# Optimization experiments

Hardware: AMD Instinct MI355X
Metric: run time of the kernel (lower is better)

The kernel has to match this reference:

```python
import jax, jax.numpy as jnp
import numpy as np

H = 1024  # hidden_size == input_size


def setup_inputs() -> dict:
    key = jax.random.key(0)
    ks = jax.random.split(key, 12)
    B, T, S, I = 64, 128, 256, 1024
    sc_in = 1.0 / np.sqrt(I)
    sc_h = 1.0 / np.sqrt(H)
    return {
        "trg_emb": jax.random.normal(ks[0], (B, T, I), jnp.float32),
        "h0": jax.random.normal(ks[1], (B, H), jnp.float32),
        "c0": jax.random.normal(ks[2], (B, H), jnp.float32),
        "ctx": jax.random.normal(ks[3], (B, S, H), jnp.float32),
        "src_len": jax.random.randint(ks[4], (B,), 1, S + 1, jnp.int32),
        # nn.LSTM params (gate order i, f, g, o)
        "W_ih": jax.random.uniform(ks[5], (4 * H, I), jnp.float32, -sc_h, sc_h),
        "W_hh": jax.random.uniform(ks[6], (4 * H, H), jnp.float32, -sc_h, sc_h),
        "b_ih": jax.random.uniform(ks[7], (4 * H,), jnp.float32, -sc_h, sc_h),
        "b_hh": jax.random.uniform(ks[8], (4 * H,), jnp.float32, -sc_h, sc_h),
        # GlobalAttention (Luong general): linear_in (H->H), linear_out (2H->H), no bias
        "W_in": jax.random.uniform(ks[9], (H, H), jnp.float32, -sc_h, sc_h),
        "W_out": jax.random.uniform(ks[10], (H, 2 * H), jnp.float32, -sc_h, sc_h),
    }


def _lstm_scan(trg_emb, h0, c0, W_ih, W_hh, b_ih, b_hh):
    # Precompute input contributions for all steps: [B,T,4H] -> scan over T
    x_gates = jnp.einsum('bti,gi->btg', trg_emb, W_ih) + b_ih + b_hh

    def step(carry, xg):
        h, c = carry
        gates = xg + h @ W_hh.T  # [B,4H]
        i, f, g, o = jnp.split(gates, 4, axis=-1)
        c = jax.nn.sigmoid(f) * c + jax.nn.sigmoid(i) * jnp.tanh(g)
        h = jax.nn.sigmoid(o) * jnp.tanh(c)
        return (h, c), h

    (hT, cT), hs = jax.lax.scan(step, (h0, c0), jnp.swapaxes(x_gates, 0, 1))
    return jnp.swapaxes(hs, 0, 1), hT, cT  # [B,T,H], [B,H], [B,H]


def reference(trg_emb, h0, c0, ctx, src_len, W_ih, W_hh, b_ih, b_hh, W_in, W_out):
    # input_feed=False: LSTM recurrence is independent of attention -> run once,
    # then batch the global attention over all T timesteps (same math as the loop).
    lstm_out, hT, cT = _lstm_scan(trg_emb, h0, c0, W_ih, W_hh, b_ih, b_hh)

    q = jnp.einsum('bth,gh->btg', lstm_out, W_in)          # linear_in
    scores = jnp.einsum('bth,bsh->bts', q, ctx)            # [B,T,S]
    mask = jnp.arange(ctx.shape[1])[None, None, :] < src_len[:, None, None]
    scores = jnp.where(mask, scores, -jnp.inf)
    attn = jax.nn.softmax(scores, axis=-1)                 # att_dropout=0
    context = jnp.einsum('bts,bsh->bth', attn, ctx)        # [B,T,H]
    h_tilde = jnp.tanh(
        jnp.einsum('btc,hc->bth', jnp.concatenate([context, lstm_out], axis=-1), W_out)
    )  # [B,T,H]
    return h_tilde, (hT[None], cT[None])
```

## Files before the change

### kernel.cpp

```cpp
#include <hip/hip_runtime.h>
#include <math.h>

#define BB 64
#define TT 128
#define SS 256
#define HHH 1024

typedef unsigned short u16;
typedef unsigned int u32;
typedef unsigned long long u64t;
typedef __bf16 bf16x8 __attribute__((ext_vector_type(8)));
typedef float f32x4 __attribute__((ext_vector_type(4)));
typedef u16 u16x8 __attribute__((ext_vector_type(8)));

__device__ __forceinline__ float sigmoidf_(float x) { return 1.0f / (1.0f + expf(-x)); }
__device__ __forceinline__ u16 f2bf(float f) {
    __bf16 h = (__bf16)f;
    return __builtin_bit_cast(u16, h);
}
__device__ __forceinline__ float b2f(u16 u) {
    return __builtin_bit_cast(float, (u32)u << 16);
}
template <typename OT>
__device__ __forceinline__ void stout(OT* p, float v) {
    if constexpr (sizeof(OT) == 2) *p = f2bf(v); else *p = v;
}
__device__ __forceinline__ void astore(u64t* p, u64t v) {
    __hip_atomic_store(p, v, __ATOMIC_RELAXED, __HIP_MEMORY_SCOPE_AGENT);
}
__device__ __forceinline__ int afetchadd(int* p) {
    return __hip_atomic_fetch_add(p, 1, __ATOMIC_RELAXED, __HIP_MEMORY_SCOPE_AGENT);
}
__device__ __forceinline__ int aload32(const int* p) {
    return __hip_atomic_load(p, __ATOMIC_RELAXED, __HIP_MEMORY_SCOPE_AGENT);
}
__device__ __forceinline__ void astore32(int* p, int v) {
    __hip_atomic_store(p, v, __ATOMIC_RELAXED, __HIP_MEMORY_SCOPE_AGENT);
}
#define GLOAD16(gsrc, ldst)                                                      \
    __builtin_amdgcn_global_load_lds(                                            \
        (const __attribute__((address_space(1))) unsigned int*)(const void*)(gsrc), \
        (__attribute__((address_space(3))) unsigned int*)(void*)(ldst), 16, 0, 0)

__global__ __launch_bounds__(256) void convert_all(
    const float* __restrict__ trg, const float* __restrict__ wih,
    const float* __restrict__ win, const float* __restrict__ wout,
    u16* __restrict__ trg16, u16* __restrict__ wih16,
    u16* __restrict__ win16, u16* __restrict__ wout16)
{
    int b = blockIdx.x;
    const float* in;
    u16* out;
    long base;
    if (b < 4096)      { in = trg;  out = trg16;  base = (long)b * 2048; }
    else if (b < 6144) { in = wih;  out = wih16;  base = (long)(b - 4096) * 2048; }
    else if (b < 6656) { in = win;  out = win16;  base = (long)(b - 6144) * 2048; }
    else               { in = wout; out = wout16; base = (long)(b - 6656) * 2048; }
    long i = base + (long)threadIdx.x * 8;
    float4 a = *(const float4*)(in + i);
    float4 c = *(const float4*)(in + i + 4);
    u16x8 o;
    o[0] = f2bf(a.x); o[1] = f2bf(a.y); o[2] = f2bf(a.z); o[3] = f2bf(a.w);
    o[4] = f2bf(c.x); o[5] = f2bf(c.y); o[6] = f2bf(c.z); o[7] = f2bf(c.w);
    *(u16x8*)(out + i) = o;
}

__global__ __launch_bounds__(128) void wfrag_build(const float* __restrict__ W,
                                                   u16* __restrict__ WF) {
    const int w = blockIdx.x, kq = blockIdx.y, bid = blockIdx.z;
    const int t = threadIdx.x;
    const int rh = t >> 6, lane = t & 63;
    const int rowp = bid * 32 + rh * 16 + (lane & 15);
    const int g = rowp & 3, jrow = rowp >> 2;
    const int k = kq * 256 + w * 32 + (lane >> 4) * 8;
    const float* src = W + ((size_t)(g * 1024 + jrow) << 10) + k;
    float4 v0 = *(const float4*)src;
    float4 v1 = *(const float4*)(src + 4);
    float vv[8] = {v0.x, v0.y, v0.z, v0.w, v1.x, v1.y, v1.z, v1.w};
    u16x8 hi, lo;
#pragma unroll
    for (int i = 0; i < 8; ++i) {
        u16 h = f2bf(vv[i]);
        hi[i] = h;
        lo[i] = f2bf(vv[i] - b2f(h));
    }
    size_t fr = ((((size_t)bid * 4 + kq) * 8 + w) * 2 + rh) * 2;
    *(u16x8*)(WF + fr * 512 + (size_t)lane * 8) = hi;
    *(u16x8*)(WF + (fr + 1) * 512 + (size_t)lane * 8) = lo;
}

__global__ __launch_bounds__(256) void h0frag(const float* __restrict__ h0,
                                              u16* __restrict__ slot) {
    int i = blockIdx.x * 256 + threadIdx.x;
    int b = i >> 7, jg = i & 127;
    int j = jg << 3;
    const float* src = h0 + ((size_t)b << 10) + j;
    float4 v0 = *(const float4*)src;
    float4 v1 = *(const float4*)(src + 4);
    float vv[8] = {v0.x, v0.y, v0.z, v0.w, v1.x, v1.y, v1.z, v1.w};
    u16x8 hi, lo;
#pragma unroll
    for (int e = 0; e < 8; ++e) {
        u16 h = f2bf(vv[e]);
        hi[e] = h;
        lo[e] = f2bf(vv[e] - b2f(h));
    }
    int g = b >> 4, bl = b & 15;
    int kq = j >> 8, w = (j >> 5) & 7, tr = (j >> 3) & 3;
    int lane = tr * 16 + bl;
    size_t base = (size_t)g * 32768 + (size_t)((kq * 8 + w) * 2) * 512 + (size_t)lane * 8;
    *(u16x8*)(slot + base) = hi;
    *(u16x8*)(slot + base + 512) = lo;
}

template <bool TANH, bool XGT, typename OT>
__global__ __launch_bounds__(256) void gemm_mfma_bt(
    const u16* __restrict__ A0, const u16* __restrict__ A1,
    const u16* __restrict__ B, OT* __restrict__ C,
    int M, int N, int K, int KA0,
    const float* __restrict__ bias0, const float* __restrict__ bias1)
{
    __shared__ uint4 As4[512];
    __shared__ uint4 Bs4[512];
    u16* As = (u16*)As4;
    u16* Bs = (u16*)Bs4;
    const int tid = threadIdx.x;
    const int l = tid & 63;
    const int w = tid >> 6;
    const int wm = w >> 1, wn = w & 1;
    const int tc = l & 15, tr8 = (l >> 4) << 3;
    const int m0 = blockIdx.y << 7, n0 = blockIdx.x << 7;
    f32x4 acc[4][4] = {};

    for (int k0 = 0; k0 < K; k0 += 32) {
        const u16* Ap = (k0 < KA0) ? A0 : A1;
        const int koff = (k0 < KA0) ? k0 : k0 - KA0;
#pragma unroll
        for (int r = 0; r < 2; ++r) {
            int u = tid + (r << 8);
            int row = u >> 2, q = u & 3;
            size_t arow;
            if (XGT) {
                int rr = m0 + row;
                arow = (size_t)((rr & 63) * 128 + (rr >> 6));
            } else {
                arow = (size_t)(m0 + row);
            }
            GLOAD16(Ap + arow * KA0 + koff + (q << 3), &As4[u]);
            GLOAD16(B + (size_t)(n0 + row) * K + k0 + (q << 3), &Bs4[u]);
        }
        __syncthreads();
        bf16x8 bfr[4];
#pragma unroll
        for (int j = 0; j < 4; ++j)
            bfr[j] = *(const bf16x8*)(Bs + ((wn << 6) + (j << 4) + tc) * 32 + tr8);
#pragma unroll
        for (int i = 0; i < 4; ++i) {
            bf16x8 af = *(const bf16x8*)(As + ((wm << 6) + (i << 4) + tc) * 32 + tr8);
#pragma unroll
            for (int j = 0; j < 4; ++j)
                acc[i][j] = __builtin_amdgcn_mfma_f32_16x16x32_bf16(af, bfr[j], acc[i][j], 0, 0, 0);
        }
        __syncthreads();
    }
#pragma unroll
    for (int j = 0; j < 4; ++j) {
        const int col = n0 + (wn << 6) + (j << 4) + tc;
        const float bias = XGT ? (bias0[col] + bias1[col]) : 0.0f;
#pragma unroll
        for (int i = 0; i < 4; ++i) {
#pragma unroll
            for (int v = 0; v < 4; ++v) {
                int r = m0 + (wm << 6) + (i << 4) + ((l >> 4) << 2) + v;
                float val = acc[i][j][v];
                if (XGT) {
                    int newr = ((col & 1023) << 2) | (col >> 10);
                    ((float*)C)[(size_t)(r >> 6) * 262144 + (size_t)newr * 64 + (r & 63)] = val + bias;
                } else {
                    if (TANH) val = tanhf(val);
                    stout(&C[(size_t)r * N + col], val);
                }
            }
        }
    }
}

__global__ __launch_bounds__(512) void lstm_scan10(
    const float* __restrict__ xgt, const u16* __restrict__ WF,
    const float* __restrict__ c0,
    const u16* __restrict__ h0s, u16* __restrict__ ring,
    float* __restrict__ hT, float* __restrict__ cT,
    u16* __restrict__ lstm16, int* __restrict__ bar)
{
    __shared__ float red[4][64][17];
    __shared__ __align__(8) u16 tileh[16][16];
    __shared__ __align__(8) u16 tilel[16][16];
    const int tid = threadIdx.x;
    const int bid = blockIdx.x;
    const int g = bid >> 6;
    const int ib = bid & 63;
    const int kg = tid >> 6, l = tid & 63;
    const int kq = kg & 3, rh = kg >> 2;
    const int j0 = ib << 4;
    const int ebl = tid & 15;
    const int ejl = (tid >> 4) & 15;

    bf16x8 wfh[2][8], wfl[2][8];
#pragma unroll
    for (int rt = 0; rt < 2; ++rt) {
        const int R16 = ib * 4 + rh * 2 + rt;
        const int bw = R16 >> 1, rhw = R16 & 1;
#pragma unroll
        for (int w = 0; w < 8; ++w) {
            size_t fr = ((((size_t)bw * 4 + kq) * 8 + w) * 2 + rhw) * 2;
            wfh[rt][w] = *(const bf16x8*)(WF + fr * 512 + (size_t)l * 8);
            wfl[rt][w] = *(const bf16x8*)(WF + (fr + 1) * 512 + (size_t)l * 8);
        }
    }
    float cv = 0.0f;
    if (tid < 256) cv = c0[(size_t)(g * 16 + ebl) * 1024 + j0 + ejl];

    float xgvA[4] = {}, xgvB[4] = {};
    if (tid < 256) {
#pragma unroll
        for (int g2 = 0; g2 < 4; ++g2)
            xgvA[g2] = xgt[(size_t)(((j0 + ejl) << 2) + g2) * 64 + g * 16 + ebl];
    }

    const int kqs = ib >> 4, ws = (ib >> 1) & 7;
    int* const gbar = bar + (g << 9);

    for (int t = 0; t < 128; ++t) {
        const u16* hin = ((t == 0) ? h0s : (ring + (size_t)(t - 1) * 131072)) + (size_t)g * 32768;
        u16* hout = ring + (size_t)t * 131072 + (size_t)g * 32768;

        if (t < 127 && tid < 256) {
#pragma unroll
            for (int g2 = 0; g2 < 4; ++g2)
                xgvB[g2] = xgt[(size_t)(t + 1) * 262144 +
                               (size_t)(((j0 + ejl) << 2) + g2) * 64 + g * 16 + ebl];
        }

        f32x4 acc[2] = {};
        bf16x8 hbA[2], hbB[2];
#define LDW(HB, W)                                                                  \
        {                                                                           \
            size_t fb = (size_t)((kq * 8 + (W)) * 2) * 512 + (size_t)l * 8;         \
            HB[0] = *(const bf16x8*)(hin + fb);                                     \
            HB[1] = *(const bf16x8*)(hin + fb + 512);                               \
        }
        LDW(hbA, 0)
#pragma unroll
        for (int w = 0; w < 8; w += 2) {
            LDW(hbB, w + 1)
#pragma unroll
            for (int rt = 0; rt < 2; ++rt) {
                acc[rt] = __builtin_amdgcn_mfma_f32_16x16x32_bf16(wfh[rt][w], hbA[0], acc[rt], 0, 0, 0);
                acc[rt] = __builtin_amdgcn_mfma_f32_16x16x32_bf16(wfh[rt][w], hbA[1], acc[rt], 0, 0, 0);
                acc[rt] = __builtin_amdgcn_mfma_f32_16x16x32_bf16(wfl[rt][w], hbA[0], acc[rt], 0, 0, 0);
            }
            if (w + 2 < 8) LDW(hbA, w + 2)
#pragma unroll
            for (int rt = 0; rt < 2; ++rt) {
                acc[rt] = __builtin_amdgcn_mfma_f32_16x16x32_bf16(wfh[rt][w + 1], hbB[0], acc[rt], 0, 0, 0);
                acc[rt] = __builtin_amdgcn_mfma_f32_16x16x32_bf16(wfh[rt][w + 1], hbB[1], acc[rt], 0, 0, 0);
                acc[rt] = __builtin_amdgcn_mfma_f32_16x16x32_bf16(wfl[rt][w + 1], hbB[0], acc[rt], 0, 0, 0);
            }
        }
#undef LDW

#pragma unroll
        for (int rt = 0; rt < 2; ++rt)
#pragma unroll
            for (int v = 0; v < 4; ++v)
                red[kq][(rh << 5) + (rt << 4) + ((l >> 4) << 2) + v][l & 15] = acc[rt][v];
        __syncthreads();

        if (tid < 256) {
            float gate[4];
#pragma unroll
            for (int g2 = 0; g2 < 4; ++g2) {
                int rr = (ejl << 2) + g2;
                gate[g2] = red[0][rr][ebl] + red[1][rr][ebl] +
                           red[2][rr][ebl] + red[3][rr][ebl] + xgvA[g2];
            }
            float ii = sigmoidf_(gate[0]);
            float ff = sigmoidf_(gate[1]);
            float gg = tanhf(gate[2]);
            float oo = sigmoidf_(gate[3]);
            float cn = ff * cv + ii * gg;
            float hn = oo * tanhf(cn);
            cv = cn;
            u16 hh = f2bf(hn);
            tileh[ebl][ejl] = hh;
            tilel[ebl][ejl] = f2bf(hn - b2f(hh));
            if (t == 127) {
                hT[(size_t)(g * 16 + ebl) * 1024 + j0 + ejl] = hn;
                cT[(size_t)(g * 16 + ebl) * 1024 + j0 + ejl] = cn;
            }
        }
        __syncthreads();

        if (tid < 128) {
            const int plane = tid >> 6, rem = tid & 63;
            const int b2 = rem >> 2, half = (rem >> 1) & 1, qq = rem & 1;
            const int lane = ((ib & 1) * 2 + half) * 16 + b2;
            const u16* tp = plane ? &tilel[b2][half * 8 + qq * 4] : &tileh[b2][half * 8 + qq * 4];
            size_t a16 = (size_t)(((kqs * 8 + ws) * 2 + plane)) * 512 + (size_t)lane * 8 + qq * 4;
            astore((u64t*)(hout + a16), *(const u64t*)tp);
            if (plane == 0) {
                int qj = rem & 3;
                *(u64t*)(lstm16 + ((size_t)(g * 16 + b2) * 128 + t) * 1024 + j0 + qj * 4) =
                    *(const u64t*)&tileh[b2][qj * 4];
            }
        }

        if (t < 127) {
            __syncthreads();
            if (tid == 0) {
                const int leaf = ib & 7;
                int a = afetchadd(&gbar[leaf * 16]);
                if ((a & 7) == 7) {
                    int r = afetchadd(&gbar[128]);
                    if ((r & 7) == 7) astore32(&gbar[136], t + 1);
                    while (aload32(&gbar[136]) < t + 1) __builtin_amdgcn_s_sleep(1);
                    astore32(&gbar[144 + leaf * 16], t + 1);
                } else {
                    while (aload32(&gbar[144 + leaf * 16]) < t + 1)
                        __builtin_amdgcn_s_sleep(1);
                }
            }
            __syncthreads();
#pragma unroll
            for (int g2 = 0; g2 < 4; ++g2) xgvA[g2] = xgvB[g2];
        }
    }
}

__global__ __launch_bounds__(256) void scores_mfma(
    const float* __restrict__ q, const float* __restrict__ ctx,
    float* __restrict__ C)
{
    __shared__ u16 Ahi[4096], Alo[4096], Bhi[4096], Blo[4096];
    const int tid = threadIdx.x;
    const int l = tid & 63, w = tid >> 6;
    const int wm = w >> 1, wn = w & 1;
    const int tc = l & 15, tr8 = (l >> 4) << 3;
    const int b = blockIdx.z, n0 = blockIdx.x << 7;
    const float* A = q + (size_t)b * 131072;
    const float* B = ctx + (size_t)b * 262144;
    f32x4 acc[4][4] = {};

    for (int k0 = 0; k0 < 1024; k0 += 32) {
#pragma unroll
        for (int r = 0; r < 4; ++r) {
            int flat = r * 256 + tid;
            int row = flat >> 3, kq = (flat & 7) << 2;
            int o = row * 32 + kq;
            float4 va = *(const float4*)(A + (size_t)row * 1024 + k0 + kq);
            u16 a0 = f2bf(va.x), a1 = f2bf(va.y), a2 = f2bf(va.z), a3 = f2bf(va.w);
            *(ushort4*)&Ahi[o] = (ushort4){a0, a1, a2, a3};
            *(ushort4*)&Alo[o] = (ushort4){f2bf(va.x - b2f(a0)), f2bf(va.y - b2f(a1)),
                                           f2bf(va.z - b2f(a2)), f2bf(va.w - b2f(a3))};
            float4 vb = *(const float4*)(B + (size_t)(n0 + row) * 1024 + k0 + kq);
            u16 g0 = f2bf(vb.x), g1 = f2bf(vb.y), g2 = f2bf(vb.z), g3 = f2bf(vb.w);
            *(ushort4*)&Bhi[o] = (ushort4){g0, g1, g2, g3};
            *(ushort4*)&Blo[o] = (ushort4){f2bf(vb.x - b2f(g0)), f2bf(vb.y - b2f(g1)),
                                           f2bf(vb.z - b2f(g2)), f2bf(vb.w - b2f(g3))};
        }
        __syncthreads();
        bf16x8 bh[4], bl[4];
#pragma unroll
        for (int j = 0; j < 4; ++j) {
            int o = ((wn << 6) + (j << 4) + tc) * 32 + tr8;
            bh[j] = *(const bf16x8*)(Bhi + o);
            bl[j] = *(const bf16x8*)(Blo + o);
        }
#pragma unroll
        for (int i = 0; i < 4; ++i) {
            int o = ((wm << 6) + (i << 4) + tc) * 32 + tr8;
            bf16x8 ah = *(const bf16x8*)(Ahi + o);
            bf16x8 al = *(const bf16x8*)(Alo + o);
#pragma unroll
            for (int j = 0; j < 4; ++j) {
                acc[i][j] = __builtin_amdgcn_mfma_f32_16x16x32_bf16(ah, bh[j], acc[i][j], 0, 0, 0);
                acc[i][j] = __builtin_amdgcn_mfma_f32_16x16x32_bf16(ah, bl[j], acc[i][j], 0, 0, 0);
                acc[i][j] = __builtin_amdgcn_mfma_f32_16x16x32_bf16(al, bh[j], acc[i][j], 0, 0, 0);
            }
        }
        __syncthreads();
    }
#pragma unroll
    for (int j = 0; j < 4; ++j) {
        int col = n0 + (wn << 6) + (j << 4) + tc;
#pragma unroll
        for (int i = 0; i < 4; ++i)
#pragma unroll
            for (int v = 0; v < 4; ++v) {
                int r = (wm << 6) + (i << 4) + ((l >> 4) << 2) + v;
                C[(size_t)b * 32768 + (size_t)r * 256 + col] = acc[i][j][v];
            }
    }
}

__global__ __launch_bounds__(256) void softmax_mask16(
    const float* __restrict__ scores, const int* __restrict__ src_len,
    u16* __restrict__ attn16)
{
    __shared__ float red[4];
    const int b = blockIdx.y, t = blockIdx.x, s = threadIdx.x;
    const float* row = scores + ((long)b * TT + t) * SS;
    const int L = src_len[b];
    float v = (s < L) ? row[s] : -INFINITY;
    float m = v;
#pragma unroll
    for (int o = 32; o >= 1; o >>= 1) m = fmaxf(m, __shfl_xor(m, o));
    if ((s & 63) == 0) red[s >> 6] = m;
    __syncthreads();
    m = fmaxf(fmaxf(red[0], red[1]), fmaxf(red[2], red[3]));
    __syncthreads();
    float e = (s < L) ? expf(v - m) : 0.0f;
    float sum = e;
#pragma unroll
    for (int o = 32; o >= 1; o >>= 1) sum += __shfl_xor(sum, o);
    if ((s & 63) == 0) red[s >> 6] = sum;
    __syncthreads();
    sum = red[0] + red[1] + red[2] + red[3];
    attn16[((long)b * TT + t) * SS + s] = f2bf(e / sum);
}

__global__ __launch_bounds__(256) void ctxattn_mfma(
    const u16* __restrict__ attn16, const float* __restrict__ ctx,
    u16* __restrict__ ctxout16)
{
    __shared__ u16 As[4096];
    __shared__ u16 Bs[128][40];
    const int tid = threadIdx.x;
    const int l = tid & 63, w = tid >> 6;
    const int wm = w >> 1, wn = w & 1;
    const int tc = l & 15, tr8 = (l >> 4) << 3;
    const int b = blockIdx.z, n0 = blockIdx.x << 7;
    f32x4 acc[4][4] = {};

    for (int k0 = 0; k0 < 256; k0 += 32) {
        {
            int row = tid >> 1, off = (tid & 1) << 4;
            const u16* src = attn16 + (size_t)b * 32768 + (size_t)row * 256 + k0 + off;
            *(uint4*)&As[row * 32 + off] = *(const uint4*)src;
            *(uint4*)&As[row * 32 + off + 8] = *(const uint4*)(src + 8);
        }
#pragma unroll
        for (int p = 0; p < 4; ++p) {
            int flat = p * 256 + tid;
            int s = flat >> 5, hc = flat & 31;
            float4 v = *(const float4*)(ctx + (size_t)b * 262144 +
                                        (size_t)(k0 + s) * 1024 + n0 + (hc << 2));
            Bs[(hc << 2) + 0][s] = f2bf(v.x);
            Bs[(hc << 2) + 1][s] = f2bf(v.y);
            Bs[(hc << 2) + 2][s] = f2bf(v.z);
            Bs[(hc << 2) + 3][s] = f2bf(v.w);
        }
        __syncthreads();
        bf16x8 bfr[4];
#pragma unroll
        for (int j = 0; j < 4; ++j)
            bfr[j] = *(const bf16x8*)&Bs[(wn << 6) + (j << 4) + tc][tr8];
#pragma unroll
        for (int i = 0; i < 4; ++i) {
            bf16x8 af = *(const bf16x8*)(As + ((wm << 6) + (i << 4) + tc) * 32 + tr8);
#pragma unroll
            for (int j = 0; j < 4; ++j)
                acc[i][j] = __builtin_amdgcn_mfma_f32_16x16x32_bf16(af, bfr[j], acc[i][j], 0, 0, 0);
        }
        __syncthreads();
    }
#pragma unroll
    for (int j = 0; j < 4; ++j) {
        int col = n0 + (wn << 6) + (j << 4) + tc;
#pragma unroll
        for (int i = 0; i < 4; ++i)
#pragma unroll
            for (int v = 0; v < 4; ++v) {
                int r = (wm << 6) + (i << 4) + ((l >> 4) << 2) + v;
                ctxout16[((size_t)b * 128 + r) * 1024 + col] = f2bf(acc[i][j][v]);
            }
    }
}

extern "C" void kernel_launch(void* const* d_in, const int* in_sizes, int n_in,
                              void* d_out, int out_size, void* d_ws, size_t ws_size,
                              hipStream_t stream)
{
    const float* trg_emb = (const float*)d_in[0];
    const float* h0      = (const float*)d_in[1];
    const float* c0      = (const float*)d_in[2];
    const float* ctx     = (const float*)d_in[3];
    const int*   src_len = (const int*)d_in[4];
    const float* W_ih    = (const float*)d_in[5];
    const float* W_hh    = (const float*)d_in[6];
    const float* b_ih    = (const float*)d_in[7];
    const float* b_hh    = (const float*)d_in[8];
    const float* W_in    = (const float*)d_in[9];
    const float* W_out   = (const float*)d_in[10];

    float* out = (float*)d_out;
    float* h_tilde = out;
    float* hT = out + (size_t)BB * TT * HHH;
    float* cT = hT + (size_t)BB * HHH;

    char* w = (char*)d_ws;
    auto take = [&](size_t bytes) { void* p = w; w += (bytes + 255) & ~(size_t)255; return p; };
    char* base0 = w;
    u16* trg16  = (u16*)take(8388608ull * 2);
    u16* Wih16  = (u16*)take(4194304ull * 2);
    take(8388608ull);
    u16* ring   = (u16*)base0;
    u16* h0s    = (u16*)take(262144ull);
    u16* Win16  = (u16*)take(1048576ull * 2);
    u16* Wout16 = (u16*)take(2097152ull * 2);
    u16* lstm16 = (u16*)take(8388608ull * 2);
    u16* WF     = (u16*)take(16777216ull);
    int* bar    = (int*)take(8192);
    char* regionB = w;
    float* xgt = (float*)take(33554432ull * 4);
    float* q        = (float*)regionB;
    float* scores   = (float*)(regionB + 33554432ull);
    u16*   attn16   = (u16*)(regionB + 41943040ull);
    u16*   ctxout16 = (u16*)(regionB + 46137344ull);

    hipMemsetAsync(bar, 0, 8192, stream);

    convert_all<<<7680, 256, 0, stream>>>(trg_emb, W_ih, W_in, W_out,
                                          trg16, Wih16, Win16, Wout16);
    wfrag_build<<<dim3(8, 4, 128), 128, 0, stream>>>(W_hh, WF);
    h0frag<<<32, 256, 0, stream>>>(h0, h0s);

    gemm_mfma_bt<false, true, float><<<dim3(32, 64), 256, 0, stream>>>(
        trg16, trg16, Wih16, xgt, 8192, 4096, 1024, 1024, b_ih, b_hh);

    lstm_scan10<<<256, 512, 0, stream>>>(xgt, WF, c0, h0s, ring,
                                         hT, cT, lstm16, bar);

    gemm_mfma_bt<false, false, float><<<dim3(8, 64), 256, 0, stream>>>(
        lstm16, lstm16, Win16, q, 8192, 1024, 1024, 1024, nullptr, nullptr);

    scores_mfma<<<dim3(2, 1, 64), 256, 0, stream>>>(q, ctx, scores);

    softmax_mask16<<<dim3(TT, BB, 1), 256, 0, stream>>>(scores, src_len, attn16);

    ctxattn_mfma<<<dim3(8, 1, 64), 256, 0, stream>>>(attn16, ctx, ctxout16);

    gemm_mfma_bt<true, false, float><<<dim3(8, 64), 256, 0, stream>>>(
        ctxout16, lstm16, Wout16, h_tilde, 8192, 1024, 2048, 1024, nullptr, nullptr);
}
```

Measured before the change: 1.015 ms.

## Fuse input-gate projection into persistent LSTM scan using LDS-resident W_ih fragments

Drops the separate large x@W_ih GEMM and its fp32 xgt buffer. Each persistent LSTM block now loads its 128KB slice of bf16 W_ih fragments into shared memory once. Every step it computes that step's input contribution with extra MFMAs on pre-swizzled trg fragments, and the bias is added at the gate stage. This trades a standalone GEMM plus a large write/read of xgt for extra per-step work on the serial recurrence critical path and much higher LDS use, which may cut occupancy.

```diff
diff --git a/kernel.cpp b/kernel.cpp
--- a/kernel.cpp
+++ b/kernel.cpp
@@ -42,20 +42,16 @@
         (const __attribute__((address_space(1))) unsigned int*)(const void*)(gsrc), \
         (__attribute__((address_space(3))) unsigned int*)(void*)(ldst), 16, 0, 0)
 
-__global__ __launch_bounds__(256) void convert_all(
-    const float* __restrict__ trg, const float* __restrict__ wih,
+__global__ __launch_bounds__(256) void convert_winout(
     const float* __restrict__ win, const float* __restrict__ wout,
-    u16* __restrict__ trg16, u16* __restrict__ wih16,
     u16* __restrict__ win16, u16* __restrict__ wout16)
 {
     int b = blockIdx.x;
     const float* in;
     u16* out;
     long base;
-    if (b < 4096)      { in = trg;  out = trg16;  base = (long)b * 2048; }
-    else if (b < 6144) { in = wih;  out = wih16;  base = (long)(b - 4096) * 2048; }
-    else if (b < 6656) { in = win;  out = win16;  base = (long)(b - 6144) * 2048; }
-    else               { in = wout; out = wout16; base = (long)(b - 6656) * 2048; }
+    if (b < 512) { in = win;  out = win16;  base = (long)b * 2048; }
+    else         { in = wout; out = wout16; base = (long)(b - 512) * 2048; }
     long i = base + (long)threadIdx.x * 8;
     float4 a = *(const float4*)(in + i);
     float4 c = *(const float4*)(in + i + 4);
@@ -89,6 +85,46 @@
     *(u16x8*)(WF + (fr + 1) * 512 + (size_t)lane * 8) = lo;
 }
 
+__global__ __launch_bounds__(256) void wihfrag_build(const float* __restrict__ Wih,
+                                                     u16* __restrict__ WihF) {
+    const int w = blockIdx.x, kq = blockIdx.y, ib = blockIdx.z;
+    const int sub = threadIdx.x >> 6;
+    const int lane = threadIdx.x & 63;
+    const int newr = ib * 64 + sub * 16 + (lane & 15);
+    const int j = newr >> 2, g = newr & 3;
+    const int k = kq * 256 + w * 32 + (lane >> 4) * 8;
+    const float* src = Wih + ((size_t)(g * 1024 + j) << 10) + k;
+    float4 v0 = *(const float4*)src;
+    float4 v1 = *(const float4*)(src + 4);
+    float vv[8] = {v0.x, v0.y, v0.z, v0.w, v1.x, v1.y, v1.z, v1.w};
+    u16x8 hi;
+#pragma unroll
+    for (int i = 0; i < 8; ++i) hi[i] = f2bf(vv[i]);
+    size_t fr = (((size_t)ib * 4 + kq) * 8 + w) * 4 + sub;
+    *(u16x8*)(WihF + fr * 512 + (size_t)lane * 8) = hi;
+}
+
+__global__ __launch_bounds__(256) void trgfrag_build(const float* __restrict__ trg,
+                                                     u16* __restrict__ trgF) {
+    int i = blockIdx.x * 256 + threadIdx.x;
+    int b = i >> 14;
+    int rem = i & 16383;
+    int t = rem >> 7, jg = rem & 127;
+    int k = jg << 3;
+    const float* src = trg + ((size_t)b * 128 + t) * 1024 + k;
+    float4 v0 = *(const float4*)src;
+    float4 v1 = *(const float4*)(src + 4);
+    float vv[8] = {v0.x, v0.y, v0.z, v0.w, v1.x, v1.y, v1.z, v1.w};
+    u16x8 hi;
+#pragma unroll
+    for (int e = 0; e < 8; ++e) hi[e] = f2bf(vv[e]);
+    int g = b >> 4, bl = b & 15;
+    int kq = k >> 8, w = (k >> 5) & 7, tr = (k >> 3) & 3;
+    int lane = tr * 16 + bl;
+    size_t fr = (((size_t)t * 4 + g) * 4 + kq) * 8 + w;
+    *(u16x8*)(trgF + fr * 512 + (size_t)lane * 8) = hi;
+}
+
 __global__ __launch_bounds__(256) void h0frag(const float* __restrict__ h0,
                                               u16* __restrict__ slot) {
     int i = blockIdx.x * 256 + threadIdx.x;
@@ -113,12 +149,11 @@
     *(u16x8*)(slot + base + 512) = lo;
 }
 
-template <bool TANH, bool XGT, typename OT>
+template <bool TANH, typename OT>
 __global__ __launch_bounds__(256) void gemm_mfma_bt(
     const u16* __restrict__ A0, const u16* __restrict__ A1,
     const u16* __restrict__ B, OT* __restrict__ C,
-    int M, int N, int K, int KA0,
-    const float* __restrict__ bias0, const float* __restrict__ bias1)
+    int M, int N, int K, int KA0)
 {
     __shared__ uint4 As4[512];
     __shared__ uint4 Bs4[512];
@@ -139,14 +174,7 @@
         for (int r = 0; r < 2; ++r) {
             int u = tid + (r << 8);
             int row = u >> 2, q = u & 3;
-            size_t arow;
-            if (XGT) {
-                int rr = m0 + row;
-                arow = (size_t)((rr & 63) * 128 + (rr >> 6));
-            } else {
-                arow = (size_t)(m0 + row);
-            }
-            GLOAD16(Ap + arow * KA0 + koff + (q << 3), &As4[u]);
+            GLOAD16(Ap + (size_t)(m0 + row) * KA0 + koff + (q << 3), &As4[u]);
             GLOAD16(B + (size_t)(n0 + row) * K + k0 + (q << 3), &Bs4[u]);
         }
         __syncthreads();
@@ -166,32 +194,28 @@
 #pragma unroll
     for (int j = 0; j < 4; ++j) {
         const int col = n0 + (wn << 6) + (j << 4) + tc;
-        const float bias = XGT ? (bias0[col] + bias1[col]) : 0.0f;
 #pragma unroll
         for (int i = 0; i < 4; ++i) {
 #pragma unroll
             for (int v = 0; v < 4; ++v) {
                 int r = m0 + (wm << 6) + (i << 4) + ((l >> 4) << 2) + v;
                 float val = acc[i][j][v];
-                if (XGT) {
-                    int newr = ((col & 1023) << 2) | (col >> 10);
-                    ((float*)C)[(size_t)(r >> 6) * 262144 + (size_t)newr * 64 + (r & 63)] = val + bias;
-                } else {
-                    if (TANH) val = tanhf(val);
-                    stout(&C[(size_t)r * N + col], val);
-                }
-            }
-        }
-    }
-}
-
-__global__ __launch_bounds__(512) void lstm_scan10(
-    const float* __restrict__ xgt, const u16* __restrict__ WF,
-    const float* __restrict__ c0,
+                if (TANH) val = tanhf(val);
+                stout(&C[(size_t)r * N + col], val);
+            }
+        }
+    }
+}
+
+__global__ __launch_bounds__(512) void lstm_scan11(
+    const u16* __restrict__ trgF, const u16* __restrict__ WihF,
+    const u16* __restrict__ WF, const float* __restrict__ c0,
+    const float* __restrict__ b_ih, const float* __restrict__ b_hh,
     const u16* __restrict__ h0s, u16* __restrict__ ring,
     float* __restrict__ hT, float* __restrict__ cT,
     u16* __restrict__ lstm16, int* __restrict__ bar)
 {
+    __shared__ u16 WihL[65536];
     __shared__ float red[4][64][17];
     __shared__ __align__(8) u16 tileh[16][16];
     __shared__ __align__(8) u16 tilel[16][16];
@@ -205,6 +229,12 @@
     const int ebl = tid & 15;
     const int ejl = (tid >> 4) & 15;
 
+    {
+        const uint4* src = (const uint4*)(WihF + (size_t)ib * 65536);
+        uint4* dst = (uint4*)WihL;
+        for (int i = tid; i < 8192; i += 512) dst[i] = src[i];
+    }
+
     bf16x8 wfh[2][8], wfl[2][8];
 #pragma unroll
     for (int rt = 0; rt < 2; ++rt) {
@@ -217,15 +247,14 @@
             wfl[rt][w] = *(const bf16x8*)(WF + (fr + 1) * 512 + (size_t)l * 8);
         }
     }
-    float cv = 0.0f;
-    if (tid < 256) cv = c0[(size_t)(g * 16 + ebl) * 1024 + j0 + ejl];
-
-    float xgvA[4] = {}, xgvB[4] = {};
+    float cv = 0.0f, biasv[4] = {};
     if (tid < 256) {
+        cv = c0[(size_t)(g * 16 + ebl) * 1024 + j0 + ejl];
 #pragma unroll
         for (int g2 = 0; g2 < 4; ++g2)
-            xgvA[g2] = xgt[(size_t)(((j0 + ejl) << 2) + g2) * 64 + g * 16 + ebl];
-    }
+            biasv[g2] = b_ih[g2 * 1024 + j0 + ejl] + b_hh[g2 * 1024 + j0 + ejl];
+    }
+    __syncthreads();
 
     const int kqs = ib >> 4, ws = (ib >> 1) & 7;
     int* const gbar = bar + (g << 9);
@@ -234,12 +263,11 @@
         const u16* hin = ((t == 0) ? h0s : (ring + (size_t)(t - 1) * 131072)) + (size_t)g * 32768;
         u16* hout = ring + (size_t)t * 131072 + (size_t)g * 32768;
 
-        if (t < 127 && tid < 256) {
-#pragma unroll
-            for (int g2 = 0; g2 < 4; ++g2)
-                xgvB[g2] = xgt[(size_t)(t + 1) * 262144 +
-                               (size_t)(((j0 + ejl) << 2) + g2) * 64 + g * 16 + ebl];
-        }
+        const u16* tf = trgF + ((((size_t)t * 4 + g) * 4 + kq) * 8) * 512;
+        bf16x8 tb[8];
+#pragma unroll
+        for (int w = 0; w < 8; ++w)
+            tb[w] = *(const bf16x8*)(tf + (size_t)w * 512 + l * 8);
 
         f32x4 acc[2] = {};
         bf16x8 hbA[2], hbB[2];
@@ -250,6 +278,17 @@
             HB[1] = *(const bf16x8*)(hin + fb + 512);                               \
         }
         LDW(hbA, 0)
+
+#pragma unroll
+        for (int w = 0; w < 8; ++w) {
+#pragma unroll
+            for (int rt = 0; rt < 2; ++rt) {
+                const u16* wp = WihL + ((((size_t)kq * 8 + w) * 4) + rh * 2 + rt) * 512;
+                bf16x8 wf = *(const bf16x8*)(wp + (size_t)l * 8);
+                acc[rt] = __builtin_amdgcn_mfma_f32_16x16x32_bf16(wf, tb[w], acc[rt], 0, 0, 0);
+            }
+        }
+
 #pragma unroll
         for (int w = 0; w < 8; w += 2) {
             LDW(hbB, w + 1)
@@ -282,7 +321,7 @@
             for (int g2 = 0; g2 < 4; ++g2) {
                 int rr = (ejl << 2) + g2;
                 gate[g2] = red[0][rr][ebl] + red[1][rr][ebl] +
-                           red[2][rr][ebl] + red[3][rr][ebl] + xgvA[g2];
+                           red[2][rr][ebl] + red[3][rr][ebl] + biasv[g2];
             }
             float ii = sigmoidf_(gate[0]);
             float ff = sigmoidf_(gate[1]);
@@ -331,8 +370,6 @@
                 }
             }
             __syncthreads();
-#pragma unroll
-            for (int g2 = 0; g2 < 4; ++g2) xgvA[g2] = xgvB[g2];
         }
     }
 }
@@ -510,19 +547,16 @@
 
     char* w = (char*)d_ws;
     auto take = [&](size_t bytes) { void* p = w; w += (bytes + 255) & ~(size_t)255; return p; };
-    char* base0 = w;
-    u16* trg16  = (u16*)take(8388608ull * 2);
-    u16* Wih16  = (u16*)take(4194304ull * 2);
-    take(8388608ull);
-    u16* ring   = (u16*)base0;
+    u16* ring   = (u16*)take(33554432ull);
     u16* h0s    = (u16*)take(262144ull);
+    u16* trgF   = (u16*)take(16777216ull);
+    u16* WihF   = (u16*)take(8388608ull);
+    u16* WF     = (u16*)take(16777216ull);
+    u16* lstm16 = (u16*)take(8388608ull * 2);
     u16* Win16  = (u16*)take(1048576ull * 2);
     u16* Wout16 = (u16*)take(2097152ull * 2);
-    u16* lstm16 = (u16*)take(8388608ull * 2);
-    u16* WF     = (u16*)take(16777216ull);
     int* bar    = (int*)take(8192);
     char* regionB = w;
-    float* xgt = (float*)take(33554432ull * 4);
     float* q        = (float*)regionB;
     float* scores   = (float*)(regionB + 33554432ull);
     u16*   attn16   = (u16*)(regionB + 41943040ull);
@@ -530,19 +564,17 @@
 
     hipMemsetAsync(bar, 0, 8192, stream);
 
-    convert_all<<<7680, 256, 0, stream>>>(trg_emb, W_ih, W_in, W_out,
-                                          trg16, Wih16, Win16, Wout16);
+    convert_winout<<<1536, 256, 0, stream>>>(W_in, W_out, Win16, Wout16);
     wfrag_build<<<dim3(8, 4, 128), 128, 0, stream>>>(W_hh, WF);
+    wihfrag_build<<<dim3(8, 4, 64), 256, 0, stream>>>(W_ih, WihF);
+    trgfrag_build<<<4096, 256, 0, stream>>>(trg_emb, trgF);
     h0frag<<<32, 256, 0, stream>>>(h0, h0s);
 
-    gemm_mfma_bt<false, true, float><<<dim3(32, 64), 256, 0, stream>>>(
-        trg16, trg16, Wih16, xgt, 8192, 4096, 1024, 1024, b_ih, b_hh);
-
-    lstm_scan10<<<256, 512, 0, stream>>>(xgt, WF, c0, h0s, ring,
-                                         hT, cT, lstm16, bar);
-
-    gemm_mfma_bt<false, false, float><<<dim3(8, 64), 256, 0, stream>>>(
-        lstm16, lstm16, Win16, q, 8192, 1024, 1024, 1024, nullptr, nullptr);
+    lstm_scan11<<<256, 512, 0, stream>>>(trgF, WihF, WF, c0, b_ih, b_hh,
+                                         h0s, ring, hT, cT, lstm16, bar);
+
+    gemm_mfma_bt<false, float><<<dim3(8, 64), 256, 0, stream>>>(
+        lstm16, lstm16, Win16, q, 8192, 1024, 1024, 1024);
 
     scores_mfma<<<dim3(2, 1, 64), 256, 0, stream>>>(q, ctx, scores);
 
@@ -550,6 +582,6 @@
 
     ctxattn_mfma<<<dim3(8, 1, 64), 256, 0, stream>>>(attn16, ctx, ctxout16);
 
-    gemm_mfma_bt<true, false, float><<<dim3(8, 64), 256, 0, stream>>>(
-        ctxout16, lstm16, Wout16, h_tilde, 8192, 1024, 2048, 1024, nullptr, nullptr);
-}
+    gemm_mfma_bt<true, float><<<dim3(8, 64), 256, 0, stream>>>(
+        ctxout16, lstm16, Wout16, h_tilde, 8192, 1024, 2048, 1024);
+}
```

Measured after the change: 963.5 us. -5.0%, faster.
